# Kernel tuning notes

Hardware: AMD Instinct MI355X
Metric: run time of the kernel (lower is better)

The kernel has to match this reference:

```python
import jax, jax.numpy as jnp
import numpy as np

B, L, E, R, A = 1024, 40, 1024, 1024, 512


def setup_inputs() -> dict:
    key = jax.random.key(0)
    ks = jax.random.split(key, 20)
    s = 0.05  # weight scale to avoid gate saturation
    inp = {
        "xt": jax.random.normal(ks[0], (B, E), jnp.float32),
        "xt_mask": jnp.ones((B, 1), jnp.float32),
        "V": jax.random.normal(ks[1], (B, L, R), jnp.float32),
        "pos_feat": jax.random.normal(ks[2], (B, R), jnp.float32),
        "h1": jax.random.normal(ks[3], (1, B, R), jnp.float32),
        "c1": jax.random.normal(ks[4], (1, B, R), jnp.float32),
        "h2": jax.random.normal(ks[5], (1, B, R), jnp.float32),
        "c2": jax.random.normal(ks[6], (1, B, R), jnp.float32),
        "Wg": jax.random.normal(ks[7], (E, R), jnp.float32) * s,
        "bg": jnp.zeros((R,), jnp.float32),
        "Wi1": jax.random.normal(ks[8], (E, 4 * R), jnp.float32) * s,
        "bi1": jnp.zeros((4 * R,), jnp.float32),
        "Wa1": jax.random.normal(ks[9], (R, 4 * R), jnp.float32) * s,
        "ba1": jnp.zeros((4 * R,), jnp.float32),
        "Wh1": jax.random.normal(ks[10], (R, 4 * R), jnp.float32) * s,
        "bh1": jnp.zeros((4 * R,), jnp.float32),
        "Wi2": jax.random.normal(ks[11], (R, 4 * R), jnp.float32) * s,
        "bi2": jnp.zeros((4 * R,), jnp.float32),
        "Wa2": jax.random.normal(ks[12], (R, 4 * R), jnp.float32) * s,
        "ba2": jnp.zeros((4 * R,), jnp.float32),
        "Wh2": jax.random.normal(ks[13], (R, 4 * R), jnp.float32) * s,
        "bh2": jnp.zeros((4 * R,), jnp.float32),
        "Wv2a": jax.random.normal(ks[14], (R, A), jnp.float32) * s,
        "bv2a": jnp.zeros((A,), jnp.float32),
        "Wh2a": jax.random.normal(ks[15], (2 * R, A), jnp.float32) * s,
        "bh2a": jnp.zeros((A,), jnp.float32),
        "Wa2w": jax.random.normal(ks[16], (A, 1), jnp.float32) * s,
        "ba2w": jnp.zeros((1,), jnp.float32),
    }
    return inp


def _lstm_cell(in1, in2, h, c, Wi, bi, Wa, ba, Wh, bh, mask):
    # all_input_sums: [B, 4R]; torch gate order: i, f, o (sigmoid) then g (tanh)
    s = in1 @ Wi + bi + in2 @ Wa + ba + h @ Wh + bh
    i_g = jax.nn.sigmoid(s[:, 0 * R:1 * R])
    f_g = jax.nn.sigmoid(s[:, 1 * R:2 * R])
    o_g = jax.nn.sigmoid(s[:, 2 * R:3 * R])
    g = jnp.tanh(s[:, 3 * R:4 * R])
    c_new = f_g * c + i_g * g
    c_new = c_new * mask + c * (1.0 - mask)
    h_new = o_g * jnp.tanh(c_new)
    h_new = h_new * mask + h * (1.0 - mask)
    return h_new, c_new


def reference(xt, xt_mask, V, pos_feat, h1, c1, h2, c2,
              Wg, bg, Wi1, bi1, Wa1, ba1, Wh1, bh1,
              Wi2, bi2, Wa2, ba2, Wh2, bh2,
              Wv2a, bv2a, Wh2a, bh2a, Wa2w, ba2w):
    h1l, c1l = h1[-1], c1[-1]  # [B, R]
    h2l, c2l = h2[-1], c2[-1]
    # additive attention over L frames
    hq = jnp.concatenate([h1l, h2l], axis=1) @ Wh2a + bh2a        # [B, A]
    e = jnp.tanh(hq[:, None, :] + V @ Wv2a + bv2a) @ Wa2w + ba2w  # [B, L, 1]
    w = jax.nn.softmax(e, axis=1)                                  # softmax over L
    af = jnp.sum(w * V, axis=1)                                    # [B, R]
    # gate (dropout in eval mode -> identity)
    gate = jax.nn.relu(xt @ Wg + bg)
    gated_pos = gate * pos_feat + pos_feat
    # two-layer LSTM
    out1, c1n = _lstm_cell(xt, gated_pos, h1l, c1l, Wi1, bi1, Wa1, ba1, Wh1, bh1, xt_mask)
    out2, c2n = _lstm_cell(out1, af, h2l, c2l, Wi2, bi2, Wa2, ba2, Wh2, bh2, xt_mask)
    return (out2, out1[None], c1n[None], out2[None], c2n[None])
```

## Files before the change

### kernel.cpp

```cpp
#include <hip/hip_runtime.h>
#include <math.h>

#define BB 1024
#define LL 40
#define RR 1024

using short8 = __attribute__((ext_vector_type(8))) short;
using us8    = __attribute__((ext_vector_type(8))) unsigned short;
using f32x4  = __attribute__((ext_vector_type(4))) float;

__device__ __forceinline__ ushort f2bf(float f) {
    union { float f; unsigned u; } a; a.f = f;
    unsigned r = a.u + 0x7fffu + ((a.u >> 16) & 1u);
    return (ushort)(r >> 16);
}
__device__ __forceinline__ float bf2f(ushort u) {
    union { unsigned u; float f; } a; a.u = ((unsigned)u) << 16;
    return a.f;
}
__device__ __forceinline__ float ftanh(float x) {
    float cx = fminf(fmaxf(x, -15.f), 15.f);
    float e = __expf(2.f * cx);
    return (e - 1.f) / (e + 1.f);
}
__device__ __forceinline__ float fsigmoid(float x) {
    float cx = fminf(fmaxf(x, -30.f), 30.f);
    return 1.f / (1.f + __expf(-cx));
}

__device__ __forceinline__ void gll16(const ushort* g, ushort* l) {
    __builtin_amdgcn_global_load_lds(
        (const __attribute__((address_space(1))) void*)g,
        (__attribute__((address_space(3))) void*)l,
        16, 0, 0);
}

__global__ __launch_bounds__(256) void conv_bf16_kernel(
    const float* __restrict__ src, ushort* __restrict__ dst, int n8)
{
    const int i = blockIdx.x * 256 + threadIdx.x;
    if (i >= n8) return;
    const float4* s4 = (const float4*)(src + (size_t)i * 8);
    float4 x = s4[0], y = s4[1];
    us8 v;
    v[0] = f2bf(x.x); v[1] = f2bf(x.y); v[2] = f2bf(x.z); v[3] = f2bf(x.w);
    v[4] = f2bf(y.x); v[5] = f2bf(y.y); v[6] = f2bf(y.z); v[7] = f2bf(y.w);
    ((us8*)dst)[i] = v;
}

struct CP3 { const float* in[3]; ushort* out[3]; };
__global__ __launch_bounds__(256) void conv_bf16_batch3_kernel(CP3 p, int n8)
{
    const int z = blockIdx.y;
    const int i = blockIdx.x * 256 + threadIdx.x;
    if (i >= n8) return;
    const float4* s4 = (const float4*)(p.in[z] + (size_t)i * 8);
    float4 x = s4[0], y = s4[1];
    us8 v;
    v[0] = f2bf(x.x); v[1] = f2bf(x.y); v[2] = f2bf(x.z); v[3] = f2bf(x.w);
    v[4] = f2bf(y.x); v[5] = f2bf(y.y); v[6] = f2bf(y.z); v[7] = f2bf(y.w);
    ((us8*)p.out[z])[i] = v;
}

struct TP6 { const float* in[6]; ushort* out[6]; int N[6]; };
__global__ __launch_bounds__(256) void transpose_conv_kernel(TP6 p)
{
    const int z = blockIdx.z;
    const int Nn = p.N[z];
    const int n0 = blockIdx.x * 64;
    if (n0 >= Nn) return;
    const int k0 = blockIdx.y * 64;
    const float* in = p.in[z];
    ushort* out = p.out[z];

    __shared__ float tile[64][65];
    const int t = threadIdx.x;
    const int tx = t & 63, ty = t >> 6;
#pragma unroll
    for (int r = 0; r < 16; ++r) {
        const int row = ty * 16 + r;
        tile[row][tx] = in[(size_t)(k0 + row) * Nn + n0 + tx];
    }
    __syncthreads();
    const int n = t >> 2, kq = t & 3;
    us8 v0, v1;
#pragma unroll
    for (int j = 0; j < 8; ++j) v0[j] = f2bf(tile[kq * 16 + j][n]);
#pragma unroll
    for (int j = 0; j < 8; ++j) v1[j] = f2bf(tile[kq * 16 + 8 + j][n]);
    ushort* op = out + (size_t)(n0 + n) * 1024 + k0 + kq * 16;
    *(us8*)op = v0;
    *((us8*)op + 1) = v1;
}

template <int NP, int SK, int EPI>
__global__ __launch_bounds__(256) void gemm_gl(
    const ushort* __restrict__ A0, const ushort* __restrict__ A1, const ushort* __restrict__ A2,
    const ushort* __restrict__ W0, const ushort* __restrict__ W1, const ushort* __restrict__ W2,
    ushort* __restrict__ Cp, int M, int N,
    const float* __restrict__ hq, const float* __restrict__ bv2a,
    const float* __restrict__ Wa2w, float* __restrict__ epart)
{
    __shared__ ushort As[128 * 64];
    __shared__ ushort Bs[128 * 64];

    const int t = threadIdx.x, l = t & 63, w = t >> 6;
    const int wm = w >> 1, wn = w & 1;

    int bx, by;
    if constexpr (EPI == 2) {
        const int lin = blockIdx.y * gridDim.x + blockIdx.x;
        const int swz = (lin & 7) * 160 + (lin >> 3);
        bx = swz & 3; by = swz >> 2;
    } else { bx = blockIdx.x; by = blockIdx.y; }
    const int m0 = by * 128, n0 = bx * 128;

    const int srow = l >> 3;
    const int csw  = ((l & 7) ^ (l >> 3)) * 8;

    const int kx0 = ((0 + (l >> 4)) ^ (l & 7)) * 8;
    const int kx1 = ((4 + (l >> 4)) ^ (l & 7)) * 8;

    f32x4 acc[4][4];
#pragma unroll
    for (int i = 0; i < 4; ++i)
#pragma unroll
        for (int j = 0; j < 4; ++j) acc[i][j] = (f32x4){0.f, 0.f, 0.f, 0.f};

    const int total = NP * 16;
    const int per   = total / SK;
    const int s0v   = blockIdx.z * per;
    const int sEnd  = s0v + per;

    for (int s = s0v; s < sEnd; ++s) {
        const int p  = (NP == 1) ? 0 : (s >> 4);
        const int k0 = (s & 15) << 6;
        const ushort* Ap = (p == 0) ? A0 : ((p == 1) ? A1 : A2);
        const ushort* Wp = (p == 0) ? W0 : ((p == 1) ? W1 : W2);
#pragma unroll
        for (int j = 0; j < 4; ++j) {
            const int rb = w * 32 + j * 8;
            gll16(Ap + (size_t)(m0 + rb + srow) * 1024 + k0 + csw, &As[rb * 64]);
            gll16(Wp + (size_t)(n0 + rb + srow) * 1024 + k0 + csw, &Bs[rb * 64]);
        }
        __syncthreads();

        short8 aF[4][2], bF[4][2];
#pragma unroll
        for (int mi = 0; mi < 4; ++mi) {
            const int ro = (wm * 64 + mi * 16 + (l & 15)) * 64;
            aF[mi][0] = *(const short8*)&As[ro + kx0];
            aF[mi][1] = *(const short8*)&As[ro + kx1];
        }
#pragma unroll
        for (int ni = 0; ni < 4; ++ni) {
            const int ro = (wn * 64 + ni * 16 + (l & 15)) * 64;
            bF[ni][0] = *(const short8*)&Bs[ro + kx0];
            bF[ni][1] = *(const short8*)&Bs[ro + kx1];
        }
#pragma unroll
        for (int mi = 0; mi < 4; ++mi)
#pragma unroll
            for (int ni = 0; ni < 4; ++ni) {
                acc[mi][ni] = __builtin_amdgcn_mfma_f32_16x16x32_bf16(
                    aF[mi][0], bF[ni][0], acc[mi][ni], 0, 0, 0);
                acc[mi][ni] = __builtin_amdgcn_mfma_f32_16x16x32_bf16(
                    aF[mi][1], bF[ni][1], acc[mi][ni], 0, 0, 0);
            }
        __syncthreads();
    }

    if constexpr (EPI == 3) {
        ushort* Cz = Cp + (size_t)blockIdx.z * M * N;
#pragma unroll
        for (int ni = 0; ni < 4; ++ni) {
            const int col = n0 + wn * 64 + ni * 16 + (l & 15);
#pragma unroll
            for (int mi = 0; mi < 4; ++mi) {
                const int row = m0 + wm * 64 + mi * 16 + ((l >> 4) << 2);
#pragma unroll
                for (int r = 0; r < 4; ++r)
                    Cz[(size_t)(row + r) * N + col] = f2bf(acc[mi][ni][r]);
            }
        }
    } else if constexpr (EPI == 2) {
        float* red = (float*)As;
        float wa[4], bv[4];
        int coln[4];
#pragma unroll
        for (int ni = 0; ni < 4; ++ni) {
            coln[ni] = n0 + wn * 64 + ni * 16 + (l & 15);
            wa[ni] = Wa2w[coln[ni]];
            bv[ni] = bv2a[coln[ni]];
        }
#pragma unroll
        for (int mi = 0; mi < 4; ++mi) {
            const int rowl = wm * 64 + mi * 16 + ((l >> 4) << 2);
#pragma unroll
            for (int r = 0; r < 4; ++r) {
                const int row = m0 + rowl + r;
                const int b = row / LL;
                float v = 0.f;
#pragma unroll
                for (int ni = 0; ni < 4; ++ni) {
                    float x = acc[mi][ni][r] + hq[(size_t)b * 512 + coln[ni]] + bv[ni];
                    v += ftanh(x) * wa[ni];
                }
                v += __shfl_xor(v, 1);
                v += __shfl_xor(v, 2);
                v += __shfl_xor(v, 4);
                v += __shfl_xor(v, 8);
                if ((l & 15) == 0) red[(rowl + r) * 2 + wn] = v;
            }
        }
        __syncthreads();
        if (t < 128)
            epart[(size_t)(m0 + t) * 4 + bx] = red[t * 2] + red[t * 2 + 1];
    }
}

__global__ __launch_bounds__(256) void reduce_hq_b_kernel(
    const ushort* __restrict__ part, const float* __restrict__ bias, float* __restrict__ hq)
{
    const int i = blockIdx.x * 256 + threadIdx.x;
    float s = bias[i & 511];
#pragma unroll
    for (int z = 0; z < 8; ++z) s += bf2f(part[(size_t)z * 524288 + i]);
    hq[i] = s;
}

__global__ __launch_bounds__(256) void reduce_gate_b_kernel(
    const ushort* __restrict__ part, const float* __restrict__ bias,
    const float* __restrict__ pos, ushort* __restrict__ gpb)
{
    const int i = blockIdx.x * 256 + threadIdx.x;
    float s = bias[i & 1023];
#pragma unroll
    for (int z = 0; z < 4; ++z) s += bf2f(part[(size_t)z * 1048576 + i]);
    const float g = fmaxf(s, 0.f);
    gpb[i] = f2bf(g * pos[i] + pos[i]);
}

__global__ __launch_bounds__(256) void softmax_af_kernel(
    const float* __restrict__ epart, const ushort* __restrict__ Vb,
    const float* __restrict__ ba2w, ushort* __restrict__ afb)
{
    const int b = blockIdx.x;
    const int tid = threadIdx.x;
    __shared__ float e_raw[LL];
    __shared__ float e_exp[LL];

    if (tid < LL) {
        const float* ep = &epart[(size_t)(b * LL + tid) * 4];
        float e = ba2w[0];
#pragma unroll
        for (int c = 0; c < 4; ++c) e += ep[c];
        e_raw[tid] = e;
    }
    __syncthreads();
    float mx = -1e30f;
#pragma unroll
    for (int ll = 0; ll < LL; ++ll) mx = fmaxf(mx, e_raw[ll]);
    if (tid < LL) e_exp[tid] = __expf(e_raw[tid] - mx);
    __syncthreads();
    float sum = 0.f;
#pragma unroll
    for (int ll = 0; ll < LL; ++ll) sum += e_exp[ll];
    const float inv = 1.f / sum;

    const int r4 = tid * 4;
    const ushort* vp = &Vb[(size_t)b * LL * RR + r4];
    float a0 = 0.f, a1 = 0.f, a2 = 0.f, a3 = 0.f;
#pragma unroll 8
    for (int ll = 0; ll < LL; ++ll) {
        ushort4 v = *(const ushort4*)&vp[(size_t)ll * RR];
        const float wgt = e_exp[ll];
        a0 += wgt * bf2f(v.x); a1 += wgt * bf2f(v.y);
        a2 += wgt * bf2f(v.z); a3 += wgt * bf2f(v.w);
    }
    ushort* op = &afb[(size_t)b * RR + r4];
    op[0] = f2bf(a0 * inv); op[1] = f2bf(a1 * inv);
    op[2] = f2bf(a2 * inv); op[3] = f2bf(a3 * inv);
}

__global__ __launch_bounds__(256) void lstm_finishb_kernel(
    const ushort* __restrict__ part,
    const float* __restrict__ bi, const float* __restrict__ ba, const float* __restrict__ bh,
    const float* __restrict__ c_in, const float* __restrict__ h_in, const float* __restrict__ mask,
    float* __restrict__ h_out, float* __restrict__ h_out2,
    float* __restrict__ c_out, ushort* __restrict__ h_bf)
{
    const int i = blockIdx.x * 256 + threadIdx.x;
    const int b = i >> 10;
    const int r = i & 1023;
    float sg[4];
#pragma unroll
    for (int g = 0; g < 4; ++g) {
        const int gr = g * 1024 + r;
        float s = bi[gr] + ba[gr] + bh[gr];
#pragma unroll
        for (int z = 0; z < 4; ++z)
            s += bf2f(part[(size_t)z * 4194304 + (size_t)b * 4096 + gr]);
        sg[g] = s;
    }
    const float ig = fsigmoid(sg[0]);
    const float fg = fsigmoid(sg[1]);
    const float og = fsigmoid(sg[2]);
    const float gt = ftanh(sg[3]);
    const float m = mask[b];
    const float c = c_in[i];
    float cn = fg * c + ig * gt;
    cn = cn * m + c * (1.f - m);
    const float h = h_in[i];
    float hn = og * ftanh(cn);
    hn = hn * m + h * (1.f - m);
    h_out[i] = hn;
    if (h_out2) h_out2[i] = hn;
    c_out[i] = cn;
    if (h_bf) h_bf[i] = f2bf(hn);
}

extern "C" void kernel_launch(void* const* d_in, const int* in_sizes, int n_in,
                              void* d_out, int out_size, void* d_ws, size_t ws_size,
                              hipStream_t stream) {
    const float* xt   = (const float*)d_in[0];
    const float* mask = (const float*)d_in[1];
    const float* V    = (const float*)d_in[2];
    const float* pos  = (const float*)d_in[3];
    const float* h1   = (const float*)d_in[4];
    const float* c1   = (const float*)d_in[5];
    const float* h2   = (const float*)d_in[6];
    const float* c2   = (const float*)d_in[7];
    const float* Wg   = (const float*)d_in[8];
    const float* bg   = (const float*)d_in[9];
    const float* Wi1  = (const float*)d_in[10];
    const float* bi1  = (const float*)d_in[11];
    const float* Wa1  = (const float*)d_in[12];
    const float* ba1  = (const float*)d_in[13];
    const float* Wh1  = (const float*)d_in[14];
    const float* bh1  = (const float*)d_in[15];
    const float* Wi2  = (const float*)d_in[16];
    const float* bi2  = (const float*)d_in[17];
    const float* Wa2  = (const float*)d_in[18];
    const float* ba2  = (const float*)d_in[19];
    const float* Wh2  = (const float*)d_in[20];
    const float* bh2  = (const float*)d_in[21];
    const float* Wv2a = (const float*)d_in[22];
    const float* bv2a = (const float*)d_in[23];
    const float* Wh2a = (const float*)d_in[24];
    const float* bh2a = (const float*)d_in[25];
    const float* Wa2w = (const float*)d_in[26];
    const float* ba2w = (const float*)d_in[27];

    float* out = (float*)d_out;
    float* out2  = out;
    float* out1  = out + (size_t)BB * RR;
    float* c1n   = out + 2 * (size_t)BB * RR;
    float* out2b = out + 3 * (size_t)BB * RR;
    float* c2n   = out + 4 * (size_t)BB * RR;

    ushort* wsu = (ushort*)d_ws;
    size_t o = 0;
    ushort* Vb     = wsu + o; o += (size_t)40960 * 1024;
    ushort* Wh2aT0 = wsu + o; o += (size_t)512 * 1024;
    ushort* Wh2aT1 = wsu + o; o += (size_t)512 * 1024;
    ushort* WgT    = wsu + o; o += (size_t)1024 * 1024;
    ushort* Wv2aT  = wsu + o; o += (size_t)512 * 1024;
    ushort* Wi1T   = wsu + o; o += (size_t)4096 * 1024;
    ushort* Wa1T   = wsu + o; o += (size_t)4096 * 1024;
    ushort* Wh1T   = wsu + o; o += (size_t)4096 * 1024;
    ushort* Wi2T   = wsu + o; o += (size_t)4096 * 1024;
    ushort* Wa2T   = wsu + o; o += (size_t)4096 * 1024;
    ushort* Wh2T   = wsu + o; o += (size_t)4096 * 1024;
    ushort* xtb    = wsu + o; o += (size_t)1024 * 1024;
    ushort* h1b    = wsu + o; o += (size_t)1024 * 1024;
    ushort* h2b    = wsu + o; o += (size_t)1024 * 1024;
    ushort* gpb    = wsu + o; o += (size_t)1024 * 1024;
    ushort* afb    = wsu + o; o += (size_t)1024 * 1024;
    ushort* out1b  = wsu + o; o += (size_t)1024 * 1024;
    ushort* partSb = wsu + o; o += (size_t)8 * 1024 * 512;
    float* wsf    = (float*)(wsu + o);
    float* hqf    = wsf;
    float* epart  = hqf + 524288;
    ushort* partKb = Vb;

    const dim3 blk(256);

    conv_bf16_kernel<<<dim3(20480), blk, 0, stream>>>(V, Vb, 5242880);
    {
        CP3 p; p.in[0] = xt; p.in[1] = h1; p.in[2] = h2;
        p.out[0] = xtb; p.out[1] = h1b; p.out[2] = h2b;
        conv_bf16_batch3_kernel<<<dim3(512, 3), blk, 0, stream>>>(p, 131072);
    }
    {
        TP6 p;
        p.in[0] = Wi1; p.in[1] = Wa1; p.in[2] = Wh1;
        p.in[3] = Wi2; p.in[4] = Wa2; p.in[5] = Wh2;
        p.out[0] = Wi1T; p.out[1] = Wa1T; p.out[2] = Wh1T;
        p.out[3] = Wi2T; p.out[4] = Wa2T; p.out[5] = Wh2T;
        for (int z = 0; z < 6; ++z) p.N[z] = 4096;
        transpose_conv_kernel<<<dim3(64, 16, 6), blk, 0, stream>>>(p);
    }
    {
        TP6 p;
        p.in[0] = Wh2a; p.in[1] = Wh2a + (size_t)1024 * 512;
        p.in[2] = Wg;   p.in[3] = Wv2a;
        p.out[0] = Wh2aT0; p.out[1] = Wh2aT1; p.out[2] = WgT; p.out[3] = Wv2aT;
        p.N[0] = 512; p.N[1] = 512; p.N[2] = 1024; p.N[3] = 512;
        p.in[4] = nullptr; p.in[5] = nullptr; p.out[4] = nullptr; p.out[5] = nullptr;
        p.N[4] = 0; p.N[5] = 0;
        transpose_conv_kernel<<<dim3(16, 16, 4), blk, 0, stream>>>(p);
    }

    gemm_gl<2, 8, 3><<<dim3(4, 8, 8), blk, 0, stream>>>(
        h1b, h2b, nullptr, Wh2aT0, Wh2aT1, nullptr,
        partSb, 1024, 512, nullptr, nullptr, nullptr, nullptr);
    reduce_hq_b_kernel<<<dim3(2048), blk, 0, stream>>>(partSb, bh2a, hqf);

    gemm_gl<1, 4, 3><<<dim3(8, 8, 4), blk, 0, stream>>>(
        xtb, nullptr, nullptr, WgT, nullptr, nullptr,
        partSb, 1024, 1024, nullptr, nullptr, nullptr, nullptr);
    reduce_gate_b_kernel<<<dim3(4096), blk, 0, stream>>>(partSb, bg, pos, gpb);

    gemm_gl<1, 1, 2><<<dim3(4, 320, 1), blk, 0, stream>>>(
        Vb, nullptr, nullptr, Wv2aT, nullptr, nullptr,
        nullptr, 40960, 512, hqf, bv2a, Wa2w, epart);
    softmax_af_kernel<<<dim3(BB), blk, 0, stream>>>(epart, Vb, ba2w, afb);

    gemm_gl<3, 4, 3><<<dim3(32, 8, 4), blk, 0, stream>>>(
        xtb, gpb, h1b, Wi1T, Wa1T, Wh1T,
        partKb, 1024, 4096, nullptr, nullptr, nullptr, nullptr);
    lstm_finishb_kernel<<<dim3(4096), blk, 0, stream>>>(
        partKb, bi1, ba1, bh1, c1, h1, mask, out1, nullptr, c1n, out1b);

    gemm_gl<3, 4, 3><<<dim3(32, 8, 4), blk, 0, stream>>>(
        out1b, afb, h2b, Wi2T, Wa2T, Wh2T,
        partKb, 1024, 4096, nullptr, nullptr, nullptr, nullptr);
    lstm_finishb_kernel<<<dim3(4096), blk, 0, stream>>>(
        partKb, bi2, ba2, bh2, c2, h2, mask, out2, out2b, c2n, nullptr);
}
```

Before: 322.1 us.

## Add double-buffered 256x256 8-wave GEMM for attention and LSTM projections

Introduces a new 512-thread GEMM kernel with 256x256 tiles and double-buffered LDS. It prefetches the next K slice in quarter-stages, interleaved with MFMA compute, using vmcnt waits and raw barriers, and raises wave priority around the MFMA loop. The kernel replaces the 128x128 kernel for the large V@Wv2a attention GEMM (with its tanh/dot epilogue, now reducing over 2 column blocks) and for both LSTM gate GEMMs. The goal is more data reuse per block and memory latency hidden behind compute. In exchange it uses much more LDS (128KB), has fewer blocks, and has a more fragile synchronisation scheme.

```diff
diff --git a/kernel.cpp b/kernel.cpp
--- a/kernel.cpp
+++ b/kernel.cpp
@@ -93,31 +93,196 @@
     *((us8*)op + 1) = v1;
 }
 
-template <int NP, int SK, int EPI>
-__global__ __launch_bounds__(256) void gemm_gl(
+template <int NP, int NTZ, int EPI>
+__global__ __launch_bounds__(512) void gemm8p(
     const ushort* __restrict__ A0, const ushort* __restrict__ A1, const ushort* __restrict__ A2,
     const ushort* __restrict__ W0, const ushort* __restrict__ W1, const ushort* __restrict__ W2,
     ushort* __restrict__ Cp, int M, int N,
     const float* __restrict__ hq, const float* __restrict__ bv2a,
     const float* __restrict__ Wa2w, float* __restrict__ epart)
 {
+    __shared__ ushort As[2][256 * 64];
+    __shared__ ushort Bs[2][256 * 64];
+
+    const int t = threadIdx.x, l = t & 63, w = t >> 6;
+    const int wm = w >> 2, wn = w & 3;
+
+    int mblk, nblk, bz;
+    if constexpr (EPI == 2) {
+        const int lin = blockIdx.x;
+        const int swz = (lin & 7) * 40 + (lin >> 3);
+        nblk = swz & 1; mblk = swz >> 1; bz = 0;
+    } else {
+        mblk = blockIdx.x; nblk = blockIdx.y; bz = blockIdx.z;
+    }
+    const int m0 = mblk * 256, n0 = nblk * 256;
+
+    f32x4 acc[2][4][2][2];
+#pragma unroll
+    for (int a = 0; a < 2; ++a)
+#pragma unroll
+        for (int b = 0; b < 4; ++b)
+#pragma unroll
+            for (int c = 0; c < 2; ++c)
+#pragma unroll
+                for (int d = 0; d < 2; ++d) acc[a][b][c][d] = (f32x4){0.f, 0.f, 0.f, 0.f};
+
+    const int csw = ((l & 7) ^ (l >> 3)) * 8;
+    const int kx0 = ((0 + (l >> 4)) ^ (l & 7)) * 8;
+    const int kx1 = ((4 + (l >> 4)) ^ (l & 7)) * 8;
+
+    const int s0 = bz * NTZ;
+
+    auto stage = [&](int s, int q) {
+        const int p  = (NP == 1) ? 0 : (s >> 4);
+        const int k0 = (s & 15) << 6;
+        const ushort* src;
+        ushort* dst;
+        int x0;
+        if (q & 1) {
+            src = (p == 0) ? W0 : ((p == 1) ? W1 : W2);
+            dst = &Bs[s & 1][0]; x0 = n0;
+        } else {
+            src = (p == 0) ? A0 : ((p == 1) ? A1 : A2);
+            dst = &As[s & 1][0]; x0 = m0;
+        }
+        const int h = q >> 1;
+#pragma unroll
+        for (int j = 0; j < 2; ++j) {
+            const int rb = h * 128 + j * 64 + w * 8;
+            gll16(src + (size_t)(x0 + rb + (l >> 3)) * 1024 + k0 + csw, dst + rb * 64);
+        }
+    };
+
+    stage(s0, 0); stage(s0, 1); stage(s0, 2); stage(s0, 3);
+
+    for (int ti = 0; ti < NTZ; ++ti) {
+        const int s = s0 + ti;
+        const ushort* Ab = &As[s & 1][0];
+        const ushort* Bb = &Bs[s & 1][0];
+        const bool last = (ti == NTZ - 1);
+        if (last) {
+            asm volatile("s_waitcnt vmcnt(0)" ::: "memory");
+            __builtin_amdgcn_s_barrier();
+            asm volatile("" ::: "memory");
+        }
+#pragma unroll
+        for (int q = 0; q < 4; ++q) {
+            if (!last) {
+                stage(s + 1, q);
+                asm volatile("s_waitcnt vmcnt(4)" ::: "memory");
+            }
+            __builtin_amdgcn_s_barrier();
+            asm volatile("" ::: "memory");
+
+            const int Ah = q & 1, Bh = q >> 1;
+            short8 aF[4][2], bF[2][2];
+#pragma unroll
+            for (int fm = 0; fm < 4; ++fm) {
+                const int ro = (Ah * 128 + wm * 64 + fm * 16 + (l & 15)) * 64;
+                aF[fm][0] = *(const short8*)&Ab[ro + kx0];
+                aF[fm][1] = *(const short8*)&Ab[ro + kx1];
+            }
+#pragma unroll
+            for (int fn = 0; fn < 2; ++fn) {
+                const int co = (Bh * 128 + wn * 32 + fn * 16 + (l & 15)) * 64;
+                bF[fn][0] = *(const short8*)&Bb[co + kx0];
+                bF[fn][1] = *(const short8*)&Bb[co + kx1];
+            }
+            __builtin_amdgcn_s_setprio(1);
+#pragma unroll
+            for (int fm = 0; fm < 4; ++fm)
+#pragma unroll
+                for (int fn = 0; fn < 2; ++fn) {
+                    acc[Ah][fm][Bh][fn] = __builtin_amdgcn_mfma_f32_16x16x32_bf16(
+                        aF[fm][0], bF[fn][0], acc[Ah][fm][Bh][fn], 0, 0, 0);
+                    acc[Ah][fm][Bh][fn] = __builtin_amdgcn_mfma_f32_16x16x32_bf16(
+                        aF[fm][1], bF[fn][1], acc[Ah][fm][Bh][fn], 0, 0, 0);
+                }
+            __builtin_amdgcn_s_setprio(0);
+        }
+        asm volatile("" ::: "memory");
+        __builtin_amdgcn_s_barrier();
+        asm volatile("" ::: "memory");
+    }
+
+    if constexpr (EPI == 3) {
+        ushort* Cz = Cp + (size_t)bz * M * N;
+#pragma unroll
+        for (int fmh = 0; fmh < 2; ++fmh)
+#pragma unroll
+            for (int fm = 0; fm < 4; ++fm) {
+                const int row = m0 + fmh * 128 + wm * 64 + fm * 16 + ((l >> 4) << 2);
+#pragma unroll
+                for (int fnh = 0; fnh < 2; ++fnh)
+#pragma unroll
+                    for (int fn = 0; fn < 2; ++fn) {
+                        const int col = n0 + fnh * 128 + wn * 32 + fn * 16 + (l & 15);
+#pragma unroll
+                        for (int r = 0; r < 4; ++r)
+                            Cz[(size_t)(row + r) * N + col] = f2bf(acc[fmh][fm][fnh][fn][r]);
+                    }
+            }
+    } else if constexpr (EPI == 2) {
+        float* red = (float*)&As[0][0];
+        float wa[2][2], bv[2][2];
+        int coln[2][2];
+#pragma unroll
+        for (int fnh = 0; fnh < 2; ++fnh)
+#pragma unroll
+            for (int fn = 0; fn < 2; ++fn) {
+                coln[fnh][fn] = n0 + fnh * 128 + wn * 32 + fn * 16 + (l & 15);
+                wa[fnh][fn] = Wa2w[coln[fnh][fn]];
+                bv[fnh][fn] = bv2a[coln[fnh][fn]];
+            }
+#pragma unroll
+        for (int fmh = 0; fmh < 2; ++fmh)
+#pragma unroll
+            for (int fm = 0; fm < 4; ++fm) {
+                const int rl = fmh * 128 + wm * 64 + fm * 16 + ((l >> 4) << 2);
+#pragma unroll
+                for (int r = 0; r < 4; ++r) {
+                    const int row = m0 + rl + r;
+                    const int b = row / LL;
+                    float v = 0.f;
+#pragma unroll
+                    for (int fnh = 0; fnh < 2; ++fnh)
+#pragma unroll
+                        for (int fn = 0; fn < 2; ++fn) {
+                            float x = acc[fmh][fm][fnh][fn][r]
+                                      + hq[(size_t)b * 512 + coln[fnh][fn]] + bv[fnh][fn];
+                            v += ftanh(x) * wa[fnh][fn];
+                        }
+                    v += __shfl_xor(v, 1);
+                    v += __shfl_xor(v, 2);
+                    v += __shfl_xor(v, 4);
+                    v += __shfl_xor(v, 8);
+                    if ((l & 15) == 0) red[(rl + r) * 4 + wn] = v;
+                }
+            }
+        __syncthreads();
+        if (t < 256) {
+            float s = red[t * 4] + red[t * 4 + 1] + red[t * 4 + 2] + red[t * 4 + 3];
+            epart[(size_t)(m0 + t) * 2 + nblk] = s;
+        }
+    }
+}
+
+template <int NP, int SK>
+__global__ __launch_bounds__(256) void gemm_gl(
+    const ushort* __restrict__ A0, const ushort* __restrict__ A1, const ushort* __restrict__ A2,
+    const ushort* __restrict__ W0, const ushort* __restrict__ W1, const ushort* __restrict__ W2,
+    ushort* __restrict__ Cp, int M, int N)
+{
     __shared__ ushort As[128 * 64];
     __shared__ ushort Bs[128 * 64];
 
     const int t = threadIdx.x, l = t & 63, w = t >> 6;
     const int wm = w >> 1, wn = w & 1;
-
-    int bx, by;
-    if constexpr (EPI == 2) {
-        const int lin = blockIdx.y * gridDim.x + blockIdx.x;
-        const int swz = (lin & 7) * 160 + (lin >> 3);
-        bx = swz & 3; by = swz >> 2;
-    } else { bx = blockIdx.x; by = blockIdx.y; }
-    const int m0 = by * 128, n0 = bx * 128;
+    const int m0 = blockIdx.y * 128, n0 = blockIdx.x * 128;
 
     const int srow = l >> 3;
     const int csw  = ((l & 7) ^ (l >> 3)) * 8;
-
     const int kx0 = ((0 + (l >> 4)) ^ (l & 7)) * 8;
     const int kx1 = ((4 + (l >> 4)) ^ (l & 7)) * 8;
 
@@ -170,52 +335,17 @@
         __syncthreads();
     }
 
-    if constexpr (EPI == 3) {
-        ushort* Cz = Cp + (size_t)blockIdx.z * M * N;
-#pragma unroll
-        for (int ni = 0; ni < 4; ++ni) {
-            const int col = n0 + wn * 64 + ni * 16 + (l & 15);
-#pragma unroll
-            for (int mi = 0; mi < 4; ++mi) {
-                const int row = m0 + wm * 64 + mi * 16 + ((l >> 4) << 2);
-#pragma unroll
-                for (int r = 0; r < 4; ++r)
-                    Cz[(size_t)(row + r) * N + col] = f2bf(acc[mi][ni][r]);
-            }
-        }
-    } else if constexpr (EPI == 2) {
-        float* red = (float*)As;
-        float wa[4], bv[4];
-        int coln[4];
-#pragma unroll
-        for (int ni = 0; ni < 4; ++ni) {
-            coln[ni] = n0 + wn * 64 + ni * 16 + (l & 15);
-            wa[ni] = Wa2w[coln[ni]];
-            bv[ni] = bv2a[coln[ni]];
-        }
+    ushort* Cz = Cp + (size_t)blockIdx.z * M * N;
+#pragma unroll
+    for (int ni = 0; ni < 4; ++ni) {
+        const int col = n0 + wn * 64 + ni * 16 + (l & 15);
 #pragma unroll
         for (int mi = 0; mi < 4; ++mi) {
-            const int rowl = wm * 64 + mi * 16 + ((l >> 4) << 2);
-#pragma unroll
-            for (int r = 0; r < 4; ++r) {
-                const int row = m0 + rowl + r;
-                const int b = row / LL;
-                float v = 0.f;
-#pragma unroll
-                for (int ni = 0; ni < 4; ++ni) {
-                    float x = acc[mi][ni][r] + hq[(size_t)b * 512 + coln[ni]] + bv[ni];
-                    v += ftanh(x) * wa[ni];
-                }
-                v += __shfl_xor(v, 1);
-                v += __shfl_xor(v, 2);
-                v += __shfl_xor(v, 4);
-                v += __shfl_xor(v, 8);
-                if ((l & 15) == 0) red[(rowl + r) * 2 + wn] = v;
-            }
-        }
-        __syncthreads();
-        if (t < 128)
-            epart[(size_t)(m0 + t) * 4 + bx] = red[t * 2] + red[t * 2 + 1];
+            const int row = m0 + wm * 64 + mi * 16 + ((l >> 4) << 2);
+#pragma unroll
+            for (int r = 0; r < 4; ++r)
+                Cz[(size_t)(row + r) * N + col] = f2bf(acc[mi][ni][r]);
+        }
     }
 }
 
@@ -251,11 +381,8 @@
     __shared__ float e_exp[LL];
 
     if (tid < LL) {
-        const float* ep = &epart[(size_t)(b * LL + tid) * 4];
-        float e = ba2w[0];
-#pragma unroll
-        for (int c = 0; c < 4; ++c) e += ep[c];
-        e_raw[tid] = e;
+        const float* ep = &epart[(size_t)(b * LL + tid) * 2];
+        e_raw[tid] = ba2w[0] + ep[0] + ep[1];
     }
     __syncthreads();
     float mx = -1e30f;
@@ -385,6 +512,7 @@
     ushort* partKb = Vb;
 
     const dim3 blk(256);
+    const dim3 blk8(512);
 
     conv_bf16_kernel<<<dim3(20480), blk, 0, stream>>>(V, Vb, 5242880);
     {
@@ -412,28 +540,26 @@
         transpose_conv_kernel<<<dim3(16, 16, 4), blk, 0, stream>>>(p);
     }
 
-    gemm_gl<2, 8, 3><<<dim3(4, 8, 8), blk, 0, stream>>>(
-        h1b, h2b, nullptr, Wh2aT0, Wh2aT1, nullptr,
-        partSb, 1024, 512, nullptr, nullptr, nullptr, nullptr);
+    gemm_gl<2, 8><<<dim3(4, 8, 8), blk, 0, stream>>>(
+        h1b, h2b, nullptr, Wh2aT0, Wh2aT1, nullptr, partSb, 1024, 512);
     reduce_hq_b_kernel<<<dim3(2048), blk, 0, stream>>>(partSb, bh2a, hqf);
 
-    gemm_gl<1, 4, 3><<<dim3(8, 8, 4), blk, 0, stream>>>(
-        xtb, nullptr, nullptr, WgT, nullptr, nullptr,
-        partSb, 1024, 1024, nullptr, nullptr, nullptr, nullptr);
+    gemm_gl<1, 4><<<dim3(8, 8, 4), blk, 0, stream>>>(
+        xtb, nullptr, nullptr, WgT, nullptr, nullptr, partSb, 1024, 1024);
     reduce_gate_b_kernel<<<dim3(4096), blk, 0, stream>>>(partSb, bg, pos, gpb);
 
-    gemm_gl<1, 1, 2><<<dim3(4, 320, 1), blk, 0, stream>>>(
+    gemm8p<1, 16, 2><<<dim3(320), blk8, 0, stream>>>(
         Vb, nullptr, nullptr, Wv2aT, nullptr, nullptr,
         nullptr, 40960, 512, hqf, bv2a, Wa2w, epart);
     softmax_af_kernel<<<dim3(BB), blk, 0, stream>>>(epart, Vb, ba2w, afb);
 
-    gemm_gl<3, 4, 3><<<dim3(32, 8, 4), blk, 0, stream>>>(
+    gemm8p<3, 12, 3><<<dim3(4, 16, 4), blk8, 0, stream>>>(
         xtb, gpb, h1b, Wi1T, Wa1T, Wh1T,
         partKb, 1024, 4096, nullptr, nullptr, nullptr, nullptr);
     lstm_finishb_kernel<<<dim3(4096), blk, 0, stream>>>(
         partKb, bi1, ba1, bh1, c1, h1, mask, out1, nullptr, c1n, out1b);
 
-    gemm_gl<3, 4, 3><<<dim3(32, 8, 4), blk, 0, stream>>>(
+    gemm8p<3, 12, 3><<<dim3(4, 16, 4), blk8, 0, stream>>>(
         out1b, afb, h2b, Wi2T, Wa2T, Wh2T,
         partKb, 1024, 4096, nullptr, nullptr, nullptr, nullptr);
     lstm_finishb_kernel<<<dim3(4096), blk, 0, stream>>>(
```

Result: slower. 401.6 us (+24.7%).

## Double-buffer GEMM shared tiles with K=32 stages and prefetch next stage

Applied to the files above, without the earlier changes.

Replaces the single-buffered 128x64 K-step GEMM loop with a double-buffered 128x32 K-step loop. The next stage's global-to-LDS loads are issued before computing on the current buffer, with explicit vmcnt waits and raw barriers, so load latency overlaps with MFMA work. The swizzle pattern and fragment offsets are redone for the 32-wide rows and precomputed. The trade-off is twice as many iterations and barriers per K, with less MFMA work per barrier to hide latency behind.

```diff
diff --git a/kernel.cpp b/kernel.cpp
--- a/kernel.cpp
+++ b/kernel.cpp
@@ -94,15 +94,15 @@
 }
 
 template <int NP, int SK, int EPI>
-__global__ __launch_bounds__(256) void gemm_gl(
+__global__ __launch_bounds__(256) void gemm_db(
     const ushort* __restrict__ A0, const ushort* __restrict__ A1, const ushort* __restrict__ A2,
     const ushort* __restrict__ W0, const ushort* __restrict__ W1, const ushort* __restrict__ W2,
     ushort* __restrict__ Cp, int M, int N,
     const float* __restrict__ hq, const float* __restrict__ bv2a,
     const float* __restrict__ Wa2w, float* __restrict__ epart)
 {
-    __shared__ ushort As[128 * 64];
-    __shared__ ushort Bs[128 * 64];
+    __shared__ ushort As[2][128 * 32];
+    __shared__ ushort Bs[2][128 * 32];
 
     const int t = threadIdx.x, l = t & 63, w = t >> 6;
     const int wm = w >> 1, wn = w & 1;
@@ -115,11 +115,16 @@
     } else { bx = blockIdx.x; by = blockIdx.y; }
     const int m0 = by * 128, n0 = bx * 128;
 
-    const int srow = l >> 3;
-    const int csw  = ((l & 7) ^ (l >> 3)) * 8;
-
-    const int kx0 = ((0 + (l >> 4)) ^ (l & 7)) * 8;
-    const int kx1 = ((4 + (l >> 4)) ^ (l & 7)) * 8;
+    const int srow  = l >> 2;
+    const int schnk = ((l & 3) ^ ((l >> 3) & 3)) * 8;
+
+    int aoff[4], boff[4];
+#pragma unroll
+    for (int mi = 0; mi < 4; ++mi)
+        aoff[mi] = (wm * 64 + mi * 16 + (l & 15)) * 32 + (((l >> 4) ^ ((l >> 1) & 3)) * 8);
+#pragma unroll
+    for (int ni = 0; ni < 4; ++ni)
+        boff[ni] = (wn * 64 + ni * 16 + (l & 15)) * 32 + (((l >> 4) ^ ((l >> 1) & 3)) * 8);
 
     f32x4 acc[4][4];
 #pragma unroll
@@ -127,47 +132,53 @@
 #pragma unroll
         for (int j = 0; j < 4; ++j) acc[i][j] = (f32x4){0.f, 0.f, 0.f, 0.f};
 
-    const int total = NP * 16;
+    const int total = NP * 32;
     const int per   = total / SK;
     const int s0v   = blockIdx.z * per;
     const int sEnd  = s0v + per;
 
-    for (int s = s0v; s < sEnd; ++s) {
-        const int p  = (NP == 1) ? 0 : (s >> 4);
-        const int k0 = (s & 15) << 6;
+    auto stage = [&](int s, int buf) {
+        const int p  = (NP == 1) ? 0 : (s >> 5);
+        const int k0 = (s & 31) << 5;
         const ushort* Ap = (p == 0) ? A0 : ((p == 1) ? A1 : A2);
         const ushort* Wp = (p == 0) ? W0 : ((p == 1) ? W1 : W2);
 #pragma unroll
-        for (int j = 0; j < 4; ++j) {
-            const int rb = w * 32 + j * 8;
-            gll16(Ap + (size_t)(m0 + rb + srow) * 1024 + k0 + csw, &As[rb * 64]);
-            gll16(Wp + (size_t)(n0 + rb + srow) * 1024 + k0 + csw, &Bs[rb * 64]);
+        for (int j = 0; j < 2; ++j) {
+            const int rb = j * 64 + w * 16;
+            gll16(Ap + (size_t)(m0 + rb + srow) * 1024 + k0 + schnk, &As[buf][rb * 32]);
+            gll16(Wp + (size_t)(n0 + rb + srow) * 1024 + k0 + schnk, &Bs[buf][rb * 32]);
         }
-        __syncthreads();
-
-        short8 aF[4][2], bF[4][2];
-#pragma unroll
-        for (int mi = 0; mi < 4; ++mi) {
-            const int ro = (wm * 64 + mi * 16 + (l & 15)) * 64;
-            aF[mi][0] = *(const short8*)&As[ro + kx0];
-            aF[mi][1] = *(const short8*)&As[ro + kx1];
+    };
+
+    stage(s0v, 0);
+    int cur = 0;
+    for (int s = s0v; s < sEnd; ++s) {
+        const bool pf = (s + 1 < sEnd);
+        if (pf) {
+            stage(s + 1, cur ^ 1);
+            asm volatile("s_waitcnt vmcnt(4)" ::: "memory");
+        } else {
+            asm volatile("s_waitcnt vmcnt(0)" ::: "memory");
         }
-#pragma unroll
-        for (int ni = 0; ni < 4; ++ni) {
-            const int ro = (wn * 64 + ni * 16 + (l & 15)) * 64;
-            bF[ni][0] = *(const short8*)&Bs[ro + kx0];
-            bF[ni][1] = *(const short8*)&Bs[ro + kx1];
-        }
+        __builtin_amdgcn_s_barrier();
+        asm volatile("" ::: "memory");
+
+        short8 aF[4], bF[4];
+#pragma unroll
+        for (int mi = 0; mi < 4; ++mi) aF[mi] = *(const short8*)&As[cur][aoff[mi]];
+#pragma unroll
+        for (int ni = 0; ni < 4; ++ni) bF[ni] = *(const short8*)&Bs[cur][boff[ni]];
 #pragma unroll
         for (int mi = 0; mi < 4; ++mi)
 #pragma unroll
-            for (int ni = 0; ni < 4; ++ni) {
+            for (int ni = 0; ni < 4; ++ni)
                 acc[mi][ni] = __builtin_amdgcn_mfma_f32_16x16x32_bf16(
-                    aF[mi][0], bF[ni][0], acc[mi][ni], 0, 0, 0);
-                acc[mi][ni] = __builtin_amdgcn_mfma_f32_16x16x32_bf16(
-                    aF[mi][1], bF[ni][1], acc[mi][ni], 0, 0, 0);
-            }
-        __syncthreads();
+                    aF[mi], bF[ni], acc[mi][ni], 0, 0, 0);
+
+        asm volatile("" ::: "memory");
+        __builtin_amdgcn_s_barrier();
+        asm volatile("" ::: "memory");
+        cur ^= 1;
     }
 
     if constexpr (EPI == 3) {
@@ -184,7 +195,7 @@
             }
         }
     } else if constexpr (EPI == 2) {
-        float* red = (float*)As;
+        float* red = (float*)&As[0][0];
         float wa[4], bv[4];
         int coln[4];
 #pragma unroll
@@ -412,28 +423,28 @@
         transpose_conv_kernel<<<dim3(16, 16, 4), blk, 0, stream>>>(p);
     }
 
-    gemm_gl<2, 8, 3><<<dim3(4, 8, 8), blk, 0, stream>>>(
+    gemm_db<2, 8, 3><<<dim3(4, 8, 8), blk, 0, stream>>>(
         h1b, h2b, nullptr, Wh2aT0, Wh2aT1, nullptr,
         partSb, 1024, 512, nullptr, nullptr, nullptr, nullptr);
     reduce_hq_b_kernel<<<dim3(2048), blk, 0, stream>>>(partSb, bh2a, hqf);
 
-    gemm_gl<1, 4, 3><<<dim3(8, 8, 4), blk, 0, stream>>>(
+    gemm_db<1, 4, 3><<<dim3(8, 8, 4), blk, 0, stream>>>(
         xtb, nullptr, nullptr, WgT, nullptr, nullptr,
         partSb, 1024, 1024, nullptr, nullptr, nullptr, nullptr);
     reduce_gate_b_kernel<<<dim3(4096), blk, 0, stream>>>(partSb, bg, pos, gpb);
 
-    gemm_gl<1, 1, 2><<<dim3(4, 320, 1), blk, 0, stream>>>(
+    gemm_db<1, 1, 2><<<dim3(4, 320, 1), blk, 0, stream>>>(
         Vb, nullptr, nullptr, Wv2aT, nullptr, nullptr,
         nullptr, 40960, 512, hqf, bv2a, Wa2w, epart);
     softmax_af_kernel<<<dim3(BB), blk, 0, stream>>>(epart, Vb, ba2w, afb);
 
-    gemm_gl<3, 4, 3><<<dim3(32, 8, 4), blk, 0, stream>>>(
+    gemm_db<3, 4, 3><<<dim3(32, 8, 4), blk, 0, stream>>>(
         xtb, gpb, h1b, Wi1T, Wa1T, Wh1T,
         partKb, 1024, 4096, nullptr, nullptr, nullptr, nullptr);
     lstm_finishb_kernel<<<dim3(4096), blk, 0, stream>>>(
         partKb, bi1, ba1, bh1, c1, h1, mask, out1, nullptr, c1n, out1b);
 
-    gemm_gl<3, 4, 3><<<dim3(32, 8, 4), blk, 0, stream>>>(
+    gemm_db<3, 4, 3><<<dim3(32, 8, 4), blk, 0, stream>>>(
         out1b, afb, h2b, Wi2T, Wa2T, Wh2T,
         partKb, 1024, 4096, nullptr, nullptr, nullptr, nullptr);
     lstm_finishb_kernel<<<dim3(4096), blk, 0, stream>>>(
```

Measured after the change: 366.6 us. 1.14x slower.

## Add triple-buffered pipelined GEMM kernel for attention score computation

Applied to the files above, without the earlier changes.

Replaces the attention-score GEMM (V @ Wv2a with fused tanh/dot epilogue) with a dedicated kernel. It uses a K-step of 32, three LDS buffers, and async global-to-LDS loads issued two stages ahead. Explicit vmcnt waits and raw barriers let memory transfers overlap MFMA work. This targets latency stalls in the largest GEMM (40960x512x1024), at the cost of hand-managed waitcnt logic that could be fragile if load counts change.

```diff
diff --git a/kernel.cpp b/kernel.cpp
--- a/kernel.cpp
+++ b/kernel.cpp
@@ -93,31 +93,21 @@
     *((us8*)op + 1) = v1;
 }
 
-template <int NP, int SK, int EPI>
+template <int NP, int SK>
 __global__ __launch_bounds__(256) void gemm_gl(
     const ushort* __restrict__ A0, const ushort* __restrict__ A1, const ushort* __restrict__ A2,
     const ushort* __restrict__ W0, const ushort* __restrict__ W1, const ushort* __restrict__ W2,
-    ushort* __restrict__ Cp, int M, int N,
-    const float* __restrict__ hq, const float* __restrict__ bv2a,
-    const float* __restrict__ Wa2w, float* __restrict__ epart)
+    ushort* __restrict__ Cp, int M, int N)
 {
     __shared__ ushort As[128 * 64];
     __shared__ ushort Bs[128 * 64];
 
     const int t = threadIdx.x, l = t & 63, w = t >> 6;
     const int wm = w >> 1, wn = w & 1;
-
-    int bx, by;
-    if constexpr (EPI == 2) {
-        const int lin = blockIdx.y * gridDim.x + blockIdx.x;
-        const int swz = (lin & 7) * 160 + (lin >> 3);
-        bx = swz & 3; by = swz >> 2;
-    } else { bx = blockIdx.x; by = blockIdx.y; }
-    const int m0 = by * 128, n0 = bx * 128;
+    const int m0 = blockIdx.y * 128, n0 = blockIdx.x * 128;
 
     const int srow = l >> 3;
     const int csw  = ((l & 7) ^ (l >> 3)) * 8;
-
     const int kx0 = ((0 + (l >> 4)) ^ (l & 7)) * 8;
     const int kx1 = ((4 + (l >> 4)) ^ (l & 7)) * 8;
 
@@ -170,53 +160,130 @@
         __syncthreads();
     }
 
-    if constexpr (EPI == 3) {
-        ushort* Cz = Cp + (size_t)blockIdx.z * M * N;
-#pragma unroll
-        for (int ni = 0; ni < 4; ++ni) {
-            const int col = n0 + wn * 64 + ni * 16 + (l & 15);
-#pragma unroll
-            for (int mi = 0; mi < 4; ++mi) {
-                const int row = m0 + wm * 64 + mi * 16 + ((l >> 4) << 2);
-#pragma unroll
-                for (int r = 0; r < 4; ++r)
-                    Cz[(size_t)(row + r) * N + col] = f2bf(acc[mi][ni][r]);
+    ushort* Cz = Cp + (size_t)blockIdx.z * M * N;
+#pragma unroll
+    for (int ni = 0; ni < 4; ++ni) {
+        const int col = n0 + wn * 64 + ni * 16 + (l & 15);
+#pragma unroll
+        for (int mi = 0; mi < 4; ++mi) {
+            const int row = m0 + wm * 64 + mi * 16 + ((l >> 4) << 2);
+#pragma unroll
+            for (int r = 0; r < 4; ++r)
+                Cz[(size_t)(row + r) * N + col] = f2bf(acc[mi][ni][r]);
+        }
+    }
+}
+
+__global__ __launch_bounds__(256) void attn_tri(
+    const ushort* __restrict__ A0, const ushort* __restrict__ W0,
+    const float* __restrict__ hq, const float* __restrict__ bv2a,
+    const float* __restrict__ Wa2w, float* __restrict__ epart)
+{
+    __shared__ ushort As[3][128 * 32];
+    __shared__ ushort Bs[3][128 * 32];
+
+    const int t = threadIdx.x, l = t & 63, w = t >> 6;
+    const int wm = w >> 1, wn = w & 1;
+
+    const int lin = blockIdx.y * gridDim.x + blockIdx.x;
+    const int swz = (lin & 7) * 160 + (lin >> 3);
+    const int bx = swz & 3, by = swz >> 2;
+    const int m0 = by * 128, n0 = bx * 128;
+
+    const int srow  = l >> 2;
+    const int schnk = ((l & 3) ^ ((l >> 3) & 3)) * 8;
+
+    int aoff[4], boff[4];
+#pragma unroll
+    for (int mi = 0; mi < 4; ++mi)
+        aoff[mi] = (wm * 64 + mi * 16 + (l & 15)) * 32 + (((l >> 4) ^ ((l >> 1) & 3)) * 8);
+#pragma unroll
+    for (int ni = 0; ni < 4; ++ni)
+        boff[ni] = (wn * 64 + ni * 16 + (l & 15)) * 32 + (((l >> 4) ^ ((l >> 1) & 3)) * 8);
+
+    f32x4 acc[4][4];
+#pragma unroll
+    for (int i = 0; i < 4; ++i)
+#pragma unroll
+        for (int j = 0; j < 4; ++j) acc[i][j] = (f32x4){0.f, 0.f, 0.f, 0.f};
+
+    auto stage = [&](int s, int buf) {
+        const int k0 = s << 5;
+#pragma unroll
+        for (int j = 0; j < 2; ++j) {
+            const int rb = j * 64 + w * 16;
+            gll16(A0 + (size_t)(m0 + rb + srow) * 1024 + k0 + schnk, &As[buf][rb * 32]);
+            gll16(W0 + (size_t)(n0 + rb + srow) * 1024 + k0 + schnk, &Bs[buf][rb * 32]);
+        }
+    };
+
+    constexpr int NS = 32;
+    stage(0, 0);
+    stage(1, 1);
+    for (int s = 0; s < NS; ++s) {
+        if (s >= 1 && s + 2 < NS) {
+            __builtin_amdgcn_s_barrier();
+            asm volatile("" ::: "memory");
+        }
+        if (s + 2 < NS) {
+            stage(s + 2, (s + 2) % 3);
+            asm volatile("s_waitcnt vmcnt(8)" ::: "memory");
+        } else if (s + 1 < NS) {
+            asm volatile("s_waitcnt vmcnt(4)" ::: "memory");
+        } else {
+            asm volatile("s_waitcnt vmcnt(0)" ::: "memory");
+        }
+        __builtin_amdgcn_s_barrier();
+        asm volatile("" ::: "memory");
+
+        const ushort* Ab = &As[s % 3][0];
+        const ushort* Bb = &Bs[s % 3][0];
+        short8 aF[4], bF[4];
+#pragma unroll
+        for (int mi = 0; mi < 4; ++mi) aF[mi] = *(const short8*)&Ab[aoff[mi]];
+#pragma unroll
+        for (int ni = 0; ni < 4; ++ni) bF[ni] = *(const short8*)&Bb[boff[ni]];
+#pragma unroll
+        for (int mi = 0; mi < 4; ++mi)
+#pragma unroll
+            for (int ni = 0; ni < 4; ++ni)
+                acc[mi][ni] = __builtin_amdgcn_mfma_f32_16x16x32_bf16(
+                    aF[mi], bF[ni], acc[mi][ni], 0, 0, 0);
+    }
+
+    __syncthreads();
+    float* red = (float*)&As[0][0];
+    float wa[4], bv[4];
+    int coln[4];
+#pragma unroll
+    for (int ni = 0; ni < 4; ++ni) {
+        coln[ni] = n0 + wn * 64 + ni * 16 + (l & 15);
+        wa[ni] = Wa2w[coln[ni]];
+        bv[ni] = bv2a[coln[ni]];
+    }
+#pragma unroll
+    for (int mi = 0; mi < 4; ++mi) {
+        const int rowl = wm * 64 + mi * 16 + ((l >> 4) << 2);
+#pragma unroll
+        for (int r = 0; r < 4; ++r) {
+            const int row = m0 + rowl + r;
+            const int b = row / LL;
+            float v = 0.f;
+#pragma unroll
+            for (int ni = 0; ni < 4; ++ni) {
+                float x = acc[mi][ni][r] + hq[(size_t)b * 512 + coln[ni]] + bv[ni];
+                v += ftanh(x) * wa[ni];
             }
-        }
-    } else if constexpr (EPI == 2) {
-        float* red = (float*)As;
-        float wa[4], bv[4];
-        int coln[4];
-#pragma unroll
-        for (int ni = 0; ni < 4; ++ni) {
-            coln[ni] = n0 + wn * 64 + ni * 16 + (l & 15);
-            wa[ni] = Wa2w[coln[ni]];
-            bv[ni] = bv2a[coln[ni]];
-        }
-#pragma unroll
-        for (int mi = 0; mi < 4; ++mi) {
-            const int rowl = wm * 64 + mi * 16 + ((l >> 4) << 2);
-#pragma unroll
-            for (int r = 0; r < 4; ++r) {
-                const int row = m0 + rowl + r;
-                const int b = row / LL;
-                float v = 0.f;
-#pragma unroll
-                for (int ni = 0; ni < 4; ++ni) {
-                    float x = acc[mi][ni][r] + hq[(size_t)b * 512 + coln[ni]] + bv[ni];
-                    v += ftanh(x) * wa[ni];
-                }
-                v += __shfl_xor(v, 1);
-                v += __shfl_xor(v, 2);
-                v += __shfl_xor(v, 4);
-                v += __shfl_xor(v, 8);
-                if ((l & 15) == 0) red[(rowl + r) * 2 + wn] = v;
-            }
-        }
-        __syncthreads();
-        if (t < 128)
-            epart[(size_t)(m0 + t) * 4 + bx] = red[t * 2] + red[t * 2 + 1];
-    }
+            v += __shfl_xor(v, 1);
+            v += __shfl_xor(v, 2);
+            v += __shfl_xor(v, 4);
+            v += __shfl_xor(v, 8);
+            if ((l & 15) == 0) red[(rowl + r) * 2 + wn] = v;
+        }
+    }
+    __syncthreads();
+    if (t < 128)
+        epart[(size_t)(m0 + t) * 4 + bx] = red[t * 2] + red[t * 2 + 1];
 }
 
 __global__ __launch_bounds__(256) void reduce_hq_b_kernel(
@@ -412,30 +479,25 @@
         transpose_conv_kernel<<<dim3(16, 16, 4), blk, 0, stream>>>(p);
     }
 
-    gemm_gl<2, 8, 3><<<dim3(4, 8, 8), blk, 0, stream>>>(
-        h1b, h2b, nullptr, Wh2aT0, Wh2aT1, nullptr,
-        partSb, 1024, 512, nullptr, nullptr, nullptr, nullptr);
+    gemm_gl<2, 8><<<dim3(4, 8, 8), blk, 0, stream>>>(
+        h1b, h2b, nullptr, Wh2aT0, Wh2aT1, nullptr, partSb, 1024, 512);
     reduce_hq_b_kernel<<<dim3(2048), blk, 0, stream>>>(partSb, bh2a, hqf);
 
-    gemm_gl<1, 4, 3><<<dim3(8, 8, 4), blk, 0, stream>>>(
-        xtb, nullptr, nullptr, WgT, nullptr, nullptr,
-        partSb, 1024, 1024, nullptr, nullptr, nullptr, nullptr);
+    gemm_gl<1, 4><<<dim3(8, 8, 4), blk, 0, stream>>>(
+        xtb, nullptr, nullptr, WgT, nullptr, nullptr, partSb, 1024, 1024);
     reduce_gate_b_kernel<<<dim3(4096), blk, 0, stream>>>(partSb, bg, pos, gpb);
 
-    gemm_gl<1, 1, 2><<<dim3(4, 320, 1), blk, 0, stream>>>(
-        Vb, nullptr, nullptr, Wv2aT, nullptr, nullptr,
-        nullptr, 40960, 512, hqf, bv2a, Wa2w, epart);
+    attn_tri<<<dim3(4, 320), blk, 0, stream>>>(
+        Vb, Wv2aT, hqf, bv2a, Wa2w, epart);
     softmax_af_kernel<<<dim3(BB), blk, 0, stream>>>(epart, Vb, ba2w, afb);
 
-    gemm_gl<3, 4, 3><<<dim3(32, 8, 4), blk, 0, stream>>>(
-        xtb, gpb, h1b, Wi1T, Wa1T, Wh1T,
-        partKb, 1024, 4096, nullptr, nullptr, nullptr, nullptr);
+    gemm_gl<3, 4><<<dim3(32, 8, 4), blk, 0, stream>>>(
+        xtb, gpb, h1b, Wi1T, Wa1T, Wh1T, partKb, 1024, 4096);
     lstm_finishb_kernel<<<dim3(4096), blk, 0, stream>>>(
         partKb, bi1, ba1, bh1, c1, h1, mask, out1, nullptr, c1n, out1b);
 
-    gemm_gl<3, 4, 3><<<dim3(32, 8, 4), blk, 0, stream>>>(
-        out1b, afb, h2b, Wi2T, Wa2T, Wh2T,
-        partKb, 1024, 4096, nullptr, nullptr, nullptr, nullptr);
+    gemm_gl<3, 4><<<dim3(32, 8, 4), blk, 0, stream>>>(
+        out1b, afb, h2b, Wi2T, Wa2T, Wh2T, partKb, 1024, 4096);
     lstm_finishb_kernel<<<dim3(4096), blk, 0, stream>>>(
         partKb, bi2, ba2, bh2, c2, h2, mask, out2, out2b, c2n, nullptr);
 }
```

New measurement: 326.7 us. About the same (+1.4%).
